# Kernel optimization log

Hardware: AMD Instinct MI355X
Metric: run time of the kernel (lower is better)

Reference implementation:

```python
import jax, jax.numpy as jnp
import numpy as np

VX, VY, VT = 3.0, 3.0, 1.0
PCX, PCY, PCT = 346.0, 260.0, 200.0
GX, GY = 116, 87  # ceil(346/3), ceil(260/3)
B = 4
NSEG = B * GX * GY  # dense pillar id space (replaces torch.unique)
EPS = 1e-3  # BatchNorm1d eps


def _bn_swish(h, gamma, beta):
    # BatchNorm1d (training-mode batch stats) + Swish
    mu = jnp.mean(h, axis=0)
    var = jnp.var(h, axis=0)
    h = (h - mu) * jax.lax.rsqrt(var + EPS) * gamma + beta
    return h * jax.nn.sigmoid(h)


def _voxelize(points):
    # points: [N,5] = (batch_idx, x, y, t, polarity)
    cx = jnp.floor(points[:, 1] / VX).astype(jnp.int32)
    cy = jnp.floor(points[:, 2] / VY).astype(jnp.int32)
    bi = points[:, 0].astype(jnp.int32)
    inv = (bi * GX + cx) * GY + cy  # dense pillar id == unq_inv into dense grid
    xyz = points[:, 1:4]
    cnt = jax.ops.segment_sum(jnp.ones_like(xyz[:, 0]), inv, num_segments=NSEG)
    mean = jax.ops.segment_sum(xyz, inv, num_segments=NSEG) / jnp.maximum(cnt, 1.0)[:, None]
    f_cluster = xyz - mean[inv]
    cxy = jnp.stack([cx, cy], axis=1).astype(points.dtype)
    vsz = jnp.array([VX, VY], points.dtype)
    f_center = points[:, 1:3] - (cxy * vsz + (vsz - 1.0) / 2.0)
    feats = jnp.concatenate([points[:, 1:5], f_cluster, f_center], axis=1)  # [N,9]
    scale = jnp.array([PCX, PCY, PCT, 1.0, VX, VY, PCT, VX, VY], points.dtype)
    feats = feats / scale
    return feats[:, :4], inv, cnt  # module only keeps first 4 feature columns


def _resize_bilinear_ac(x, Ho, Wo):
    # F.interpolate(mode='bilinear', align_corners=True)
    _, _, H, W = x.shape
    ys = jnp.linspace(0.0, H - 1.0, Ho)
    xs = jnp.linspace(0.0, W - 1.0, Wo)
    y0 = jnp.floor(ys).astype(jnp.int32); y1 = jnp.minimum(y0 + 1, H - 1)
    x0 = jnp.floor(xs).astype(jnp.int32); x1 = jnp.minimum(x0 + 1, W - 1)
    wy = (ys - y0.astype(x.dtype))[None, None, :, None]
    wx = (xs - x0.astype(x.dtype))[None, None, None, :]
    xh = x[:, :, y0, :] * (1.0 - wy) + x[:, :, y1, :] * wy
    return xh[:, :, :, x0] * (1.0 - wx) + xh[:, :, :, x1] * wx


def setup_inputs() -> dict:
    key = jax.random.key(0)
    ks = jax.random.split(key, 8)
    N = 1_000_000
    b = jax.random.randint(ks[0], (N, 1), 0, B).astype(jnp.float32)
    x = jax.random.uniform(ks[1], (N, 1)) * 345.9
    y = jax.random.uniform(ks[2], (N, 1)) * 259.9
    t = jax.random.uniform(ks[3], (N, 1)) * 199.9
    p = jax.random.randint(ks[4], (N, 1), 0, 2).astype(jnp.float32)
    points = jnp.concatenate([b, x, y, t, p], axis=1)
    fus = jax.random.normal(ks[5], (B, 3, 224, 224), jnp.float32)
    W0 = jax.random.normal(ks[6], (4, 32), jnp.float32) * 0.1
    g0 = jnp.ones(32, jnp.float32); b0 = jnp.zeros(32, jnp.float32)
    W1 = jax.random.normal(ks[7], (64, 128), jnp.float32) * 0.05
    g1 = jnp.ones(128, jnp.float32); b1 = jnp.zeros(128, jnp.float32)
    return {"fus": fus, "points": points, "W0": W0, "g0": g0, "b0": b0,
            "W1": W1, "g1": g1, "b1": b1}


def reference(fus, points, W0, g0, b0, W1, g1, b1):
    feats, inv, cnt = _voxelize(points)
    # PFNLayer 0 (not last): units = 64//2 = 32, concat per-pillar max
    h0 = _bn_swish(feats @ W0, g0, b0)
    m0 = jax.ops.segment_max(h0, inv, num_segments=NSEG)
    x1 = jnp.concatenate([h0, m0[inv]], axis=1)  # [N,64]
    # PFNLayer 1 (last): units = 128, returns broadcast per-pillar max
    h1 = _bn_swish(x1 @ W1, g1, b1)
    m1 = jax.ops.segment_max(h1, inv, num_segments=NSEG)  # [NSEG,128]
    # final scatter_max over the broadcast max equals m1 on occupied pillars;
    # spconv .dense() zero-fills empty pillars
    occ = cnt > 0
    dense = jnp.where(occ[:, None], m1, 0.0)
    dense = dense.reshape(B, GX, GY, -1).transpose(0, 3, 2, 1)  # [B,C,GY,GX]
    return _resize_bilinear_ac(dense, 224, 224)
```

## Files before the change

kernel.cpp:

```cpp
#include <hip/hip_runtime.h>
#include <cmath>

#define NPTS   1000000
#define GXD    116
#define GYD    87
#define NB     4
#define NSEG   40368
#define OUTN   25690112

#define SEGBLK 4096
#define CHUNKMAX 10

#define OFF_INV    0
#define OFF_CNT    2000000
#define OFF_OFFS   2050000
#define OFF_FILL   2100000
#define OFF_STATS  2150000
#define OFF_BN0    2158500
#define OFF_FRAG   2158592
#define OFF_MINP   2170000
#define OFF_MAXP   7340000
#define OFF_SPTS   12510000

typedef __attribute__((ext_vector_type(8))) short short8v;
typedef __attribute__((ext_vector_type(4))) float float4v;

union Frag {
  unsigned u[4];
  int4 i4;
  short8v v;
};

__device__ __forceinline__ float fastrcp(float x) { return __builtin_amdgcn_rcpf(x); }
__device__ __forceinline__ float swishf(float z) { return z * fastrcp(1.0f + __expf(-z)); }
__device__ __forceinline__ unsigned fbits(float x) { return __builtin_bit_cast(unsigned, x); }
__device__ __forceinline__ float ubf(unsigned x) { return __builtin_bit_cast(float, x); }

__device__ __forceinline__ float min3f(float a, float b, float c) {
  float d; asm("v_min3_f32 %0, %1, %2, %3" : "=v"(d) : "v"(a), "v"(b), "v"(c)); return d;
}
__device__ __forceinline__ float max3f(float a, float b, float c) {
  float d; asm("v_max3_f32 %0, %1, %2, %3" : "=v"(d) : "v"(a), "v"(b), "v"(c)); return d;
}

__device__ __forceinline__ void bfsplit2(float x0, float x1, unsigned& hi, unsigned& lo) {
  unsigned h0b = fbits(x0) & 0xffff0000u;
  unsigned h1b = fbits(x1) & 0xffff0000u;
  hi = (h0b >> 16) | h1b;
  float l0 = x0 - ubf(h0b), l1 = x1 - ubf(h1b);
  lo = (fbits(l0) >> 16) | (fbits(l1) & 0xffff0000u);
}

__global__ __launch_bounds__(256) void k_init(int* __restrict__ cnt, int* __restrict__ fill,
                                              float* __restrict__ stats) {
  int i = blockIdx.x * 256 + threadIdx.x;
  if (i < NSEG) { cnt[i] = 0; fill[i] = 0; }
  if (i < 8224) stats[i] = 0.0f;
}

__global__ __launch_bounds__(256) void k_point1(const float* __restrict__ pts,
                                                int* __restrict__ inv,
                                                int* __restrict__ cnt,
                                                float* __restrict__ Sg) {
  float acc[14];
  #pragma unroll
  for (int q = 0; q < 14; ++q) acc[q] = 0.0f;
  const float i346 = 1.0f / 346.0f, i260 = 1.0f / 260.0f, i200 = 1.0f / 200.0f;
  const int stride = gridDim.x * 256;
  for (int i = blockIdx.x * 256 + threadIdx.x; i < NPTS; i += stride) {
    float b = pts[i*5];
    float4 v = *(const float4*)(pts + i*5 + 1);
    float x = v.x, y = v.y, t = v.z, p = v.w;
    int cx = (int)floorf(x / 3.0f);
    int cy = (int)floorf(y / 3.0f);
    int bi = (int)b;
    if (cx >= 0 && cx < GXD && cy >= 0 && cy < GYD && bi >= 0 && bi < NB) {
      int iv = (bi*GXD + cx)*GYD + cy;
      inv[i] = iv;
      atomicAdd(&cnt[iv], 1);
    } else {
      inv[i] = -1;
    }
    float f0 = x*i346, f1 = y*i260, f2 = t*i200, f3 = p;
    acc[0]+=f0; acc[1]+=f1; acc[2]+=f2; acc[3]+=f3;
    acc[4]+=f0*f0; acc[5]+=f0*f1; acc[6]+=f0*f2; acc[7]+=f0*f3;
    acc[8]+=f1*f1; acc[9]+=f1*f2; acc[10]+=f1*f3;
    acc[11]+=f2*f2; acc[12]+=f2*f3; acc[13]+=f3*f3;
  }
  __shared__ float lds[4*14];
  int lane = threadIdx.x & 63, wave = threadIdx.x >> 6;
  #pragma unroll
  for (int q = 0; q < 14; ++q) {
    float v = acc[q];
    #pragma unroll
    for (int d = 32; d > 0; d >>= 1) v += __shfl_down(v, d, 64);
    if (lane == 0) lds[wave*14 + q] = v;
  }
  __syncthreads();
  if (threadIdx.x < 14) {
    float v = lds[threadIdx.x] + lds[14+threadIdx.x] + lds[28+threadIdx.x] + lds[42+threadIdx.x];
    atomicAdd(&Sg[threadIdx.x], v);
  }
}

__global__ __launch_bounds__(1024) void k_scan(const int* __restrict__ cnt,
                                               int* __restrict__ offs,
                                               const float* __restrict__ S,
                                               float* __restrict__ bn0,
                                               int4* __restrict__ frag,
                                               const float* __restrict__ W0,
                                               const float* __restrict__ g0,
                                               const float* __restrict__ b0,
                                               const float* __restrict__ W1) {
  __shared__ int wtot[16];
  const int tid = threadIdx.x;
  if (tid < 32) {
    const float invN = 1.0f / (float)NPTS;
    float w0 = W0[tid], w1 = W0[32+tid], w2 = W0[64+tid], w3 = W0[96+tid];
    float mu = (S[0]*w0 + S[1]*w1 + S[2]*w2 + S[3]*w3) * invN;
    float e2 = (S[4]*w0*w0 + S[8]*w1*w1 + S[11]*w2*w2 + S[13]*w3*w3
              + 2.0f*(S[5]*w0*w1 + S[6]*w0*w2 + S[7]*w0*w3
                    + S[9]*w1*w2 + S[10]*w1*w3 + S[12]*w2*w3)) * invN;
    float var = e2 - mu*mu;
    float a = rsqrtf(var + 1e-3f) * g0[tid];
    bn0[tid] = a;
    bn0[32+tid] = b0[tid] - mu*a;
  }
  if (tid < 512) {
    const int t = tid >> 6, ln = tid & 63;
    const int qq = ln >> 4, rr = ln & 15;
    Frag fh, fl, gh, gl;
    #pragma unroll
    for (int d = 0; d < 4; ++d) {
      int row = 8*qq + 2*d, col = 16*t + rr;
      bfsplit2(W1[row*128 + col],      W1[(row+1)*128 + col],  fh.u[d], fl.u[d]);
      bfsplit2(W1[(32+row)*128 + col], W1[(33+row)*128 + col], gh.u[d], gl.u[d]);
    }
    frag[tid]        = fh.i4;
    frag[512 + tid]  = fl.i4;
    frag[1024 + tid] = gh.i4;
    frag[1536 + tid] = gl.i4;
  }
  const int CH = 40;
  const int base = tid * CH;
  int loc[CH];
  int s = 0;
  #pragma unroll
  for (int i = 0; i < CH; ++i) {
    int v = (base + i < NSEG) ? cnt[base + i] : 0;
    loc[i] = s; s += v;
  }
  int inc = s;
  const int lane = tid & 63, wv = tid >> 6;
  #pragma unroll
  for (int d = 1; d < 64; d <<= 1) {
    int t = __shfl_up(inc, d, 64);
    if (lane >= d) inc += t;
  }
  if (lane == 63) wtot[wv] = inc;
  __syncthreads();
  if (tid == 0) {
    int run = 0;
    #pragma unroll
    for (int w = 0; w < 16; ++w) { int t = wtot[w]; wtot[w] = run; run += t; }
    offs[NSEG] = run;
  }
  __syncthreads();
  int ex = wtot[wv] + (inc - s);
  #pragma unroll
  for (int i = 0; i < CH; ++i)
    if (base + i < NSEG) offs[base + i] = ex + loc[i];
}

__global__ __launch_bounds__(256) void k_scatter(const float* __restrict__ pts,
                                                 const int* __restrict__ inv,
                                                 const int* __restrict__ offs,
                                                 int* __restrict__ fill,
                                                 float4* __restrict__ sp) {
  int i = blockIdx.x * 256 + threadIdx.x;
  if (i >= NPTS) return;
  int iv = inv[i];
  if (iv < 0) return;
  float4 v = *(const float4*)(pts + i*5 + 1);
  int pos = offs[iv] + atomicAdd(&fill[iv], 1);
  sp[pos] = v;
}

__global__ __launch_bounds__(256) void k_seg(const float4* __restrict__ sp,
                                             const int* __restrict__ offs,
                                             const float* __restrict__ W0,
                                             const float* __restrict__ bn0,
                                             const int4* __restrict__ frags,
                                             float* __restrict__ minp,
                                             float* __restrict__ maxp,
                                             float* __restrict__ stats) {
  __shared__ int4 fragLDS[1536];
  __shared__ float redS[4][16][16];
  __shared__ float mnT[CHUNKMAX][129];
  __shared__ float mxT[CHUNKMAX][129];
  const int tid = threadIdx.x;
  const int wave = tid >> 6, lane = tid & 63;
  const int q = lane >> 4, r = lane & 15;

  short8v Bhi[8];
  #pragma unroll
  for (int t = 0; t < 8; ++t) {
    Frag f; f.i4 = frags[t*64 + lane];
    Bhi[t] = f.v;
  }
  for (int i = tid; i < 1536; i += 256) fragLDS[i] = frags[512 + i];

  const float i346 = 1.0f/346.0f, i260 = 1.0f/260.0f, i200 = 1.0f/200.0f;
  float wax[8], way[8], wat[8], wap[8], wc0[8];
  #pragma unroll
  for (int j = 0; j < 8; ++j) {
    int ch = 8*q + j;
    float a0 = bn0[ch];
    wax[j] = W0[ch]    * (i346 * a0);
    way[j] = W0[32+ch] * (i260 * a0);
    wat[j] = W0[64+ch] * (i200 * a0);
    wap[j] = W0[96+ch] * a0;
    wc0[j] = bn0[32+ch];
  }
  __syncthreads();

  float gsum[8], gssq[8];
  #pragma unroll
  for (int t = 0; t < 8; ++t) { gsum[t] = 0.f; gssq[t] = 0.f; }

  const int bq = NSEG / SEGBLK;
  const int br = NSEG - bq*SEGBLK;
  const int S0 = blockIdx.x*bq + min((int)blockIdx.x, br);
  const int csz = bq + (blockIdx.x < br ? 1 : 0);

  for (int si = wave; si < csz; si += 4) {
    const int s = S0 + si;
    const int off = offs[s], pend = offs[s+1];
    const int n = pend - off;
    if (n <= 0) continue;
    const int ngroups = (n + 15) >> 4;
    float m0r[8], mn[8], mx[8], su[8], sq[8];
    #pragma unroll
    for (int t = 0; t < 8; ++t) {
      m0r[t] = -1e30f; mn[t] = 1e30f; mx[t] = -1e30f; su[t] = 0.f; sq[t] = 0.f;
    }
    float4 P = sp[off + (r < n ? r : 0)];
    for (int g = 0; g < ngroups; ++g) {
      int slot1 = (g+1)*16 + r;
      float4 Pn = sp[off + (slot1 < n ? slot1 : 0)];

      float h0v[8];
      #pragma unroll
      for (int j = 0; j < 8; ++j) {
        float pre = fmaf(P.x, wax[j], fmaf(P.y, way[j], fmaf(P.z, wat[j], fmaf(P.w, wap[j], wc0[j]))));
        float h = swishf(pre);
        h0v[j] = h;
        m0r[j] = fmaxf(m0r[j], h);
      }
      Frag ah, al;
      #pragma unroll
      for (int d = 0; d < 4; ++d)
        bfsplit2(h0v[2*d], h0v[2*d+1], ah.u[d], al.u[d]);

      const int rem = n - g*16;
      #pragma unroll
      for (int t = 0; t < 8; ++t) {
        Frag fb; fb.i4 = fragLDS[t*64 + lane];
        float4v acc = {0.f, 0.f, 0.f, 0.f};
        acc = __builtin_amdgcn_mfma_f32_16x16x32_bf16(ah.v, Bhi[t], acc, 0, 0, 0);
        acc = __builtin_amdgcn_mfma_f32_16x16x32_bf16(ah.v, fb.v,   acc, 0, 0, 0);
        acc = __builtin_amdgcn_mfma_f32_16x16x32_bf16(al.v, Bhi[t], acc, 0, 0, 0);
        float z0 = acc[0], z1 = acc[1], z2 = acc[2], z3 = acc[3];
        if (rem >= 16) {
          mn[t] = min3f(z0, z1, min3f(z2, z3, mn[t]));
          mx[t] = max3f(z0, z1, max3f(z2, z3, mx[t]));
          su[t] += (z0 + z1) + (z2 + z3);
          sq[t] = fmaf(z0, z0, sq[t]); sq[t] = fmaf(z1, z1, sq[t]);
          sq[t] = fmaf(z2, z2, sq[t]); sq[t] = fmaf(z3, z3, sq[t]);
        } else {
          mn[t] = min3f(z0, z1, min3f(z2, z3, mn[t]));
          mx[t] = max3f(z0, z1, max3f(z2, z3, mx[t]));
          float zz0 = (4*q + 0 < rem) ? z0 : 0.f;
          float zz1 = (4*q + 1 < rem) ? z1 : 0.f;
          float zz2 = (4*q + 2 < rem) ? z2 : 0.f;
          float zz3 = (4*q + 3 < rem) ? z3 : 0.f;
          su[t] += (zz0 + zz1) + (zz2 + zz3);
          sq[t] = fmaf(zz0, zz0, sq[t]); sq[t] = fmaf(zz1, zz1, sq[t]);
          sq[t] = fmaf(zz2, zz2, sq[t]); sq[t] = fmaf(zz3, zz3, sq[t]);
        }
      }
      P = Pn;
    }

    #pragma unroll
    for (int j = 0; j < 8; ++j) {
      float v = m0r[j];
      v = fmaxf(v, __shfl_xor(v, 1, 64));
      v = fmaxf(v, __shfl_xor(v, 2, 64));
      v = fmaxf(v, __shfl_xor(v, 4, 64));
      v = fmaxf(v, __shfl_xor(v, 8, 64));
      m0r[j] = v;
    }
    Frag mh, ml;
    #pragma unroll
    for (int d = 0; d < 4; ++d)
      bfsplit2(m0r[2*d], m0r[2*d+1], mh.u[d], ml.u[d]);
    float c[8];
    #pragma unroll
    for (int t = 0; t < 8; ++t) {
      Frag gh; gh.i4 = fragLDS[512 + t*64 + lane];
      Frag gl; gl.i4 = fragLDS[1024 + t*64 + lane];
      float4v cacc = {0.f, 0.f, 0.f, 0.f};
      cacc = __builtin_amdgcn_mfma_f32_16x16x32_bf16(mh.v, gh.v, cacc, 0, 0, 0);
      cacc = __builtin_amdgcn_mfma_f32_16x16x32_bf16(mh.v, gl.v, cacc, 0, 0, 0);
      cacc = __builtin_amdgcn_mfma_f32_16x16x32_bf16(ml.v, gh.v, cacc, 0, 0, 0);
      c[t] = cacc[0];
    }
    #pragma unroll
    for (int t = 0; t < 8; ++t) {
      mn[t] = fminf(mn[t], __shfl_xor(mn[t], 16, 64));
      mn[t] = fminf(mn[t], __shfl_xor(mn[t], 32, 64));
      mx[t] = fmaxf(mx[t], __shfl_xor(mx[t], 16, 64));
      mx[t] = fmaxf(mx[t], __shfl_xor(mx[t], 32, 64));
      su[t] += __shfl_xor(su[t], 16, 64);
      su[t] += __shfl_xor(su[t], 32, 64);
      sq[t] += __shfl_xor(sq[t], 16, 64);
      sq[t] += __shfl_xor(sq[t], 32, 64);
      float nf = (float)n;
      gsum[t] += su[t] + nf * c[t];
      gssq[t] += sq[t] + 2.0f*c[t]*su[t] + nf*c[t]*c[t];
    }
    if (lane < 16) {
      #pragma unroll
      for (int t = 0; t < 8; ++t) {
        mnT[si][16*t + r] = mn[t] + c[t];
        mxT[si][16*t + r] = mx[t] + c[t];
      }
    }
  }

  if (lane < 16) {
    #pragma unroll
    for (int t = 0; t < 8; ++t) {
      redS[wave][r][t]     = gsum[t];
      redS[wave][r][8 + t] = gssq[t];
    }
  }
  __syncthreads();

  for (int i = tid; i < (csz << 7); i += 256) {
    int ch = i / csz, si = i - ch*csz;
    minp[ch*NSEG + S0 + si] = mnT[si][ch];
    maxp[ch*NSEG + S0 + si] = mxT[si][ch];
  }
  if (wave == 0 && lane < 16) {
    const int cpy = blockIdx.x & 15;
    float* sb = stats + 16 + 512*cpy;
    #pragma unroll
    for (int t = 0; t < 8; ++t) {
      float s0v = redS[0][r][t]   + redS[1][r][t]   + redS[2][r][t]   + redS[3][r][t];
      float q0v = redS[0][r][8+t] + redS[1][r][8+t] + redS[2][r][8+t] + redS[3][r][8+t];
      atomicAdd(&sb[16*t + r], s0v);
      atomicAdd(&sb[256 + 16*t + r], q0v);
    }
  }
}

__global__ __launch_bounds__(256) void k_plane(const float* __restrict__ minp,
                                               const float* __restrict__ maxp,
                                               const int* __restrict__ offs,
                                               const float* __restrict__ stats,
                                               const float* __restrict__ g1,
                                               const float* __restrict__ b1,
                                               float* __restrict__ out) {
  __shared__ float plane[87*117];
  __shared__ float ab[2];
  const int c = blockIdx.x & 127;
  const int b = blockIdx.x >> 7;
  const int tid = threadIdx.x;
  if (tid == 0) {
    float s = 0.f, q2 = 0.f;
    #pragma unroll
    for (int cpy = 0; cpy < 16; ++cpy) {
      s  += stats[16 + 512*cpy + c];
      q2 += stats[16 + 512*cpy + 256 + c];
    }
    const float invN = 1.0f / (float)NPTS;
    float mu = s * invN;
    float var = q2 * invN - mu*mu;
    float a = rsqrtf(var + 1e-3f) * g1[c];
    ab[0] = a;
    ab[1] = b1[c] - mu*a;
  }
  __syncthreads();
  const float a = ab[0], bb = ab[1];
  const int sBase = b * (GXD*GYD);
  const float* mnp = minp + c*NSEG + sBase;
  const float* mxp = maxp + c*NSEG + sBase;
  for (int i = tid; i < GXD*GYD; i += 256) {
    int gx = i / GYD, gy = i - gx*GYD;
    float m = 0.0f;
    int s = sBase + i;
    if (offs[s+1] - offs[s] > 0) {
      float zl = fmaf(a, mnp[i], bb);
      float zh = fmaf(a, mxp[i], bb);
      m = fmaxf(swishf(zl), swishf(zh));
    }
    plane[gy*117 + gx] = m;
  }
  __syncthreads();
  float* op = out + (size_t)blockIdx.x * (224*224);
  for (int o4 = tid; o4 < 224*56; o4 += 256) {
    int xq = o4 % 56;
    int yo = o4 / 56;
    float ys = (float)yo * (86.0f/223.0f);
    float yf = floorf(ys); int y0 = (int)yf; int y1 = min(y0+1, 86); float wy = ys - yf;
    const float* p0 = plane + y0*117;
    const float* p1 = plane + y1*117;
    float res[4];
    #pragma unroll
    for (int gph = 0; gph < 4; ++gph) {
      int xo = xq*4 + gph;
      float xs = (float)xo * (115.0f/223.0f);
      float xf = floorf(xs); int x0 = (int)xf; int x1 = min(x0+1, 115); float wx = xs - xf;
      float c0v = p0[x0]*(1.0f-wy) + p1[x0]*wy;
      float c1v = p0[x1]*(1.0f-wy) + p1[x1]*wy;
      res[gph] = c0v*(1.0f-wx) + c1v*wx;
    }
    *(float4*)&op[yo*224 + xq*4] = make_float4(res[0], res[1], res[2], res[3]);
  }
}

extern "C" void kernel_launch(void* const* d_in, const int* in_sizes, int n_in,
                              void* d_out, int out_size, void* d_ws, size_t ws_size,
                              hipStream_t stream) {
  const float* pts = (const float*)d_in[1];
  const float* W0  = (const float*)d_in[2];
  const float* g0  = (const float*)d_in[3];
  const float* b0  = (const float*)d_in[4];
  const float* W1  = (const float*)d_in[5];
  const float* g1  = (const float*)d_in[6];
  const float* b1  = (const float*)d_in[7];
  float* out = (float*)d_out;
  int*   wsi = (int*)d_ws;
  float* wsf = (float*)d_ws;

  k_init<<<158, 256, 0, stream>>>(wsi+OFF_CNT, wsi+OFF_FILL, wsf+OFF_STATS);
  k_point1<<<256, 256, 0, stream>>>(pts, wsi+OFF_INV, wsi+OFF_CNT, wsf+OFF_STATS);
  k_scan<<<1, 1024, 0, stream>>>(wsi+OFF_CNT, wsi+OFF_OFFS, wsf+OFF_STATS, wsf+OFF_BN0,
                                 (int4*)(wsf+OFF_FRAG), W0, g0, b0, W1);
  k_scatter<<<(NPTS+255)/256, 256, 0, stream>>>(pts, wsi+OFF_INV, wsi+OFF_OFFS,
                                                wsi+OFF_FILL, (float4*)(wsf+OFF_SPTS));
  k_seg<<<SEGBLK, 256, 0, stream>>>((const float4*)(wsf+OFF_SPTS), wsi+OFF_OFFS, W0,
                                    wsf+OFF_BN0, (const int4*)(wsf+OFF_FRAG),
                                    wsf+OFF_MINP, wsf+OFF_MAXP, wsf+OFF_STATS);
  k_plane<<<NB*128, 256, 0, stream>>>(wsf+OFF_MINP, wsf+OFF_MAXP, wsi+OFF_OFFS,
                                      wsf+OFF_STATS, g1, b1, out);
}
```

Measured before the change: 458.0 us.

## Assign contiguous pillars per wave, precompute layer-0 coefficients, write min/max directly

The per-pillar kernel now assigns each wave its own contiguous range of pillars (2048 blocks × 4 waves), replacing the per-block range with a strided wave loop. The LDS transpose staging and its second write-out pass are removed, so lanes store min/max straight to the channel-major global arrays. The fused layer-0 coefficients are computed once in the scan kernel and read as float4 vectors. Wave priority is raised around the MFMA loop. The direct stores are strided by NSEG per channel and no longer coalesced, which may raise global write cost.

New measurement: 434.3 us. -5.2%, faster.

```diff
diff --git a/kernel.cpp b/kernel.cpp
--- a/kernel.cpp
+++ b/kernel.cpp
@@ -8,16 +8,14 @@
 #define NSEG   40368
 #define OUTN   25690112
 
-#define SEGBLK 4096
-#define CHUNKMAX 10
-
 #define OFF_INV    0
 #define OFF_CNT    2000000
 #define OFF_OFFS   2050000
 #define OFF_FILL   2100000
 #define OFF_STATS  2150000
 #define OFF_BN0    2158500
-#define OFF_FRAG   2158592
+#define OFF_COEF   2158600
+#define OFF_FRAG   2158900
 #define OFF_MINP   2170000
 #define OFF_MAXP   7340000
 #define OFF_SPTS   12510000
@@ -107,6 +105,7 @@
                                                int* __restrict__ offs,
                                                const float* __restrict__ S,
                                                float* __restrict__ bn0,
+                                               float* __restrict__ coef,
                                                int4* __restrict__ frag,
                                                const float* __restrict__ W0,
                                                const float* __restrict__ g0,
@@ -116,6 +115,7 @@
   const int tid = threadIdx.x;
   if (tid < 32) {
     const float invN = 1.0f / (float)NPTS;
+    const float i346 = 1.0f/346.0f, i260 = 1.0f/260.0f, i200 = 1.0f/200.0f;
     float w0 = W0[tid], w1 = W0[32+tid], w2 = W0[64+tid], w3 = W0[96+tid];
     float mu = (S[0]*w0 + S[1]*w1 + S[2]*w2 + S[3]*w3) * invN;
     float e2 = (S[4]*w0*w0 + S[8]*w1*w1 + S[11]*w2*w2 + S[13]*w3*w3
@@ -125,6 +125,11 @@
     float a = rsqrtf(var + 1e-3f) * g0[tid];
     bn0[tid] = a;
     bn0[32+tid] = b0[tid] - mu*a;
+    coef[tid]        = w0 * (i346 * a);
+    coef[32 + tid]   = w1 * (i260 * a);
+    coef[64 + tid]   = w2 * (i200 * a);
+    coef[96 + tid]   = w3 * a;
+    coef[128 + tid]  = b0[tid] - mu*a;
   }
   if (tid < 512) {
     const int t = tid >> 6, ln = tid & 63;
@@ -188,16 +193,13 @@
 
 __global__ __launch_bounds__(256) void k_seg(const float4* __restrict__ sp,
                                              const int* __restrict__ offs,
-                                             const float* __restrict__ W0,
-                                             const float* __restrict__ bn0,
+                                             const float* __restrict__ coef,
                                              const int4* __restrict__ frags,
                                              float* __restrict__ minp,
                                              float* __restrict__ maxp,
                                              float* __restrict__ stats) {
   __shared__ int4 fragLDS[1536];
   __shared__ float redS[4][16][16];
-  __shared__ float mnT[CHUNKMAX][129];
-  __shared__ float mxT[CHUNKMAX][129];
   const int tid = threadIdx.x;
   const int wave = tid >> 6, lane = tid & 63;
   const int q = lane >> 4, r = lane & 15;
@@ -210,17 +212,24 @@
   }
   for (int i = tid; i < 1536; i += 256) fragLDS[i] = frags[512 + i];
 
-  const float i346 = 1.0f/346.0f, i260 = 1.0f/260.0f, i200 = 1.0f/200.0f;
+  const float4* cf = (const float4*)coef;
   float wax[8], way[8], wat[8], wap[8], wc0[8];
-  #pragma unroll
-  for (int j = 0; j < 8; ++j) {
-    int ch = 8*q + j;
-    float a0 = bn0[ch];
-    wax[j] = W0[ch]    * (i346 * a0);
-    way[j] = W0[32+ch] * (i260 * a0);
-    wat[j] = W0[64+ch] * (i200 * a0);
-    wap[j] = W0[96+ch] * a0;
-    wc0[j] = bn0[32+ch];
+  {
+    float4 a0v = cf[0*8 + 2*q], a1v = cf[0*8 + 2*q + 1];
+    float4 b0v = cf[1*8 + 2*q], b1v = cf[1*8 + 2*q + 1];
+    float4 c0v = cf[2*8 + 2*q], c1v = cf[2*8 + 2*q + 1];
+    float4 d0v = cf[3*8 + 2*q], d1v = cf[3*8 + 2*q + 1];
+    float4 e0v = cf[4*8 + 2*q], e1v = cf[4*8 + 2*q + 1];
+    wax[0]=a0v.x; wax[1]=a0v.y; wax[2]=a0v.z; wax[3]=a0v.w;
+    wax[4]=a1v.x; wax[5]=a1v.y; wax[6]=a1v.z; wax[7]=a1v.w;
+    way[0]=b0v.x; way[1]=b0v.y; way[2]=b0v.z; way[3]=b0v.w;
+    way[4]=b1v.x; way[5]=b1v.y; way[6]=b1v.z; way[7]=b1v.w;
+    wat[0]=c0v.x; wat[1]=c0v.y; wat[2]=c0v.z; wat[3]=c0v.w;
+    wat[4]=c1v.x; wat[5]=c1v.y; wat[6]=c1v.z; wat[7]=c1v.w;
+    wap[0]=d0v.x; wap[1]=d0v.y; wap[2]=d0v.z; wap[3]=d0v.w;
+    wap[4]=d1v.x; wap[5]=d1v.y; wap[6]=d1v.z; wap[7]=d1v.w;
+    wc0[0]=e0v.x; wc0[1]=e0v.y; wc0[2]=e0v.z; wc0[3]=e0v.w;
+    wc0[4]=e1v.x; wc0[5]=e1v.y; wc0[6]=e1v.z; wc0[7]=e1v.w;
   }
   __syncthreads();
 
@@ -228,13 +237,13 @@
   #pragma unroll
   for (int t = 0; t < 8; ++t) { gsum[t] = 0.f; gssq[t] = 0.f; }
 
-  const int bq = NSEG / SEGBLK;
-  const int br = NSEG - bq*SEGBLK;
-  const int S0 = blockIdx.x*bq + min((int)blockIdx.x, br);
-  const int csz = bq + (blockIdx.x < br ? 1 : 0);
-
-  for (int si = wave; si < csz; si += 4) {
-    const int s = S0 + si;
+  const int w = blockIdx.x*4 + wave;
+  const int qn = NSEG >> 13;
+  const int rm = NSEG - (qn << 13);
+  const int s0 = w*qn + (w < rm ? w : rm);
+  const int scnt = qn + (w < rm ? 1 : 0);
+
+  for (int s = s0; s < s0 + scnt; ++s) {
     const int off = offs[s], pend = offs[s+1];
     const int n = pend - off;
     if (n <= 0) continue;
@@ -263,6 +272,7 @@
         bfsplit2(h0v[2*d], h0v[2*d+1], ah.u[d], al.u[d]);
 
       const int rem = n - g*16;
+      __builtin_amdgcn_s_setprio(1);
       #pragma unroll
       for (int t = 0; t < 8; ++t) {
         Frag fb; fb.i4 = fragLDS[t*64 + lane];
@@ -289,6 +299,7 @@
           sq[t] = fmaf(zz2, zz2, sq[t]); sq[t] = fmaf(zz3, zz3, sq[t]);
         }
       }
+      __builtin_amdgcn_s_setprio(0);
       P = Pn;
     }
 
@@ -333,12 +344,11 @@
     if (lane < 16) {
       #pragma unroll
       for (int t = 0; t < 8; ++t) {
-        mnT[si][16*t + r] = mn[t] + c[t];
-        mxT[si][16*t + r] = mx[t] + c[t];
+        minp[(16*t + r)*NSEG + s] = mn[t] + c[t];
+        maxp[(16*t + r)*NSEG + s] = mx[t] + c[t];
       }
     }
   }
-
   if (lane < 16) {
     #pragma unroll
     for (int t = 0; t < 8; ++t) {
@@ -347,12 +357,6 @@
     }
   }
   __syncthreads();
-
-  for (int i = tid; i < (csz << 7); i += 256) {
-    int ch = i / csz, si = i - ch*csz;
-    minp[ch*NSEG + S0 + si] = mnT[si][ch];
-    maxp[ch*NSEG + S0 + si] = mxT[si][ch];
-  }
   if (wave == 0 && lane < 16) {
     const int cpy = blockIdx.x & 15;
     float* sb = stats + 16 + 512*cpy;
@@ -448,12 +452,12 @@
   k_init<<<158, 256, 0, stream>>>(wsi+OFF_CNT, wsi+OFF_FILL, wsf+OFF_STATS);
   k_point1<<<256, 256, 0, stream>>>(pts, wsi+OFF_INV, wsi+OFF_CNT, wsf+OFF_STATS);
   k_scan<<<1, 1024, 0, stream>>>(wsi+OFF_CNT, wsi+OFF_OFFS, wsf+OFF_STATS, wsf+OFF_BN0,
-                                 (int4*)(wsf+OFF_FRAG), W0, g0, b0, W1);
+                                 wsf+OFF_COEF, (int4*)(wsf+OFF_FRAG), W0, g0, b0, W1);
   k_scatter<<<(NPTS+255)/256, 256, 0, stream>>>(pts, wsi+OFF_INV, wsi+OFF_OFFS,
                                                 wsi+OFF_FILL, (float4*)(wsf+OFF_SPTS));
-  k_seg<<<SEGBLK, 256, 0, stream>>>((const float4*)(wsf+OFF_SPTS), wsi+OFF_OFFS, W0,
-                                    wsf+OFF_BN0, (const int4*)(wsf+OFF_FRAG),
-                                    wsf+OFF_MINP, wsf+OFF_MAXP, wsf+OFF_STATS);
+  k_seg<<<2048, 256, 0, stream>>>((const float4*)(wsf+OFF_SPTS), wsi+OFF_OFFS,
+                                  wsf+OFF_COEF, (const int4*)(wsf+OFF_FRAG),
+                                  wsf+OFF_MINP, wsf+OFF_MAXP, wsf+OFF_STATS);
   k_plane<<<NB*128, 256, 0, stream>>>(wsf+OFF_MINP, wsf+OFF_MAXP, wsi+OFF_OFFS,
                                       wsf+OFF_STATS, g1, b1, out);
 }
```
